# Optimization experiments

Hardware: AMD Instinct MI355X
Metric: run time of the kernel (lower is better)

Reference implementation:

```python
import jax, jax.numpy as jnp
import numpy as np

N = 50000
E = 800000
IN_C, HID_C, OUT_C = 128, 128, 64


def setup_inputs() -> dict:
    key = jax.random.key(0)
    ks = jax.random.split(key, 8)
    x = jax.random.normal(ks[0], (N, IN_C), dtype=jnp.float32)
    edge_index = jax.random.randint(ks[1], (2, E), 0, N, dtype=jnp.int64)
    s = lambda fan_in: 1.0 / np.sqrt(fan_in)
    W1 = jax.random.uniform(ks[2], (HID_C, IN_C), jnp.float32, -s(IN_C), s(IN_C))
    b1 = jnp.zeros((HID_C,), jnp.float32)
    W2 = jax.random.uniform(ks[3], (HID_C, HID_C), jnp.float32, -s(HID_C), s(HID_C))
    b2 = jnp.zeros((HID_C,), jnp.float32)
    Wp = jax.random.uniform(ks[4], (OUT_C, HID_C), jnp.float32, -s(HID_C), s(HID_C))
    bp = jax.random.uniform(ks[5], (OUT_C,), jnp.float32, -s(HID_C), s(HID_C))
    return {"x": x, "edge_index": edge_index, "W1": W1, "b1": b1,
            "W2": W2, "b2": b2, "Wp": Wp, "bp": bp}


def _gcn_conv(x, W, b, src, dst, n):
    # PyG GCNConv: linear transform (no bias), add self-loops, symmetric
    # normalization D^-1/2 A_hat D^-1/2, scatter-add aggregation, then bias.
    h = x @ W.T                                   # [N, out]
    loop = jnp.arange(n, dtype=src.dtype)
    s = jnp.concatenate([src, loop])              # [E+N]
    d = jnp.concatenate([dst, loop])              # [E+N]
    deg = jax.ops.segment_sum(jnp.ones_like(d, dtype=h.dtype), d, num_segments=n)
    dinv = jnp.where(deg > 0, jax.lax.rsqrt(deg), 0.0)
    norm = dinv[s] * dinv[d]                      # [E+N]
    msg = h[s] * norm[:, None]                    # gather + scale
    out = jax.ops.segment_sum(msg, d, num_segments=n)  # scatter-add to targets
    return out + b


def reference(x, edge_index, W1, b1, W2, b2, Wp, bp):
    src, dst = edge_index[0], edge_index[1]
    n = x.shape[0]
    h = jax.nn.relu(_gcn_conv(x, W1, b1, src, dst, n))
    h = jax.nn.relu(_gcn_conv(h, W2, b2, src, dst, n))
    out = h @ Wp.T + bp
    return jax.nn.relu(out)  # activation='relu'
```

## Files before the change

kernel.cpp:

```cpp
#include <hip/hip_runtime.h>

#define NN 50000
#define NE 800000
#define KD 128
#define NBUK 196
#define CHUNK 2048
#define SLACK 8192

typedef __attribute__((ext_vector_type(8))) short short8;
typedef __attribute__((ext_vector_type(4))) float f32x4;
typedef __attribute__((ext_vector_type(4))) unsigned short us4;

__device__ inline void splitbf(float x, short& h, short& l) {
    unsigned int u = __float_as_uint(x);
    unsigned int r = u + 0x8000u;
    short hh = (short)(r >> 16);
    float hf = __uint_as_float(((unsigned int)(unsigned short)hh) << 16);
    float lo = x - hf;
    unsigned int u2 = __float_as_uint(lo) + 0x8000u;
    h = hh;
    l = (short)(u2 >> 16);
}
__device__ inline unsigned short f2bf(float x) {
    unsigned int u = __float_as_uint(x);
    unsigned int r = u + 0x7FFFu + ((u >> 16) & 1u);
    return (unsigned short)(r >> 16);
}
__device__ inline float bf2f(unsigned short b) {
    return __uint_as_float(((unsigned int)b) << 16);
}

__global__ __launch_bounds__(256) void wsplit_k(
    const float* __restrict__ W1, const float* __restrict__ W2, const float* __restrict__ Wp,
    unsigned short* __restrict__ Wh, unsigned short* __restrict__ Wl,
    int* __restrict__ bcur)
{
    int t = threadIdx.x;
    if (blockIdx.x == 0 && t < NBUK) bcur[t] = 0;
    int i = blockIdx.x * 256 + t;
    float w;
    if (i < 16384) w = W1[i];
    else if (i < 32768) w = W2[i - 16384];
    else w = Wp[i - 32768];
    short h, l;
    splitbf(w, h, l);
    Wh[i] = (unsigned short)h;
    Wl[i] = (unsigned short)l;
}

__global__ __launch_bounds__(256) void bscat_k(const int* __restrict__ src, const int* __restrict__ dst,
    int* __restrict__ bcur, unsigned int* __restrict__ pairs, int e)
{
    __shared__ int h[NBUK], base[NBUK], cur[NBUK];
    int t = threadIdx.x;
    int e0 = blockIdx.x * CHUNK, e1 = min(e0 + CHUNK, e);
    for (int i = t; i < NBUK; i += 256) { h[i] = 0; cur[i] = 0; }
    __syncthreads();
    for (int i = e0 + t; i < e1; i += 256) atomicAdd(&h[dst[i] >> 8], 1);
    __syncthreads();
    for (int i = t; i < NBUK; i += 256) base[i] = h[i] ? atomicAdd(&bcur[i], h[i]) : 0;
    __syncthreads();
    for (int i = e0 + t; i < e1; i += 256) {
        int d = dst[i];
        int b = d >> 8;
        int r = atomicAdd(&cur[b], 1);
        pairs[(size_t)b * SLACK + base[b] + r] = (unsigned)src[i] | ((unsigned)(d & 255) << 16);
    }
}
__global__ __launch_bounds__(256) void bbuild_k(const unsigned int* __restrict__ pairs,
    const int* __restrict__ bcur,
    int* __restrict__ beg, int* __restrict__ endp, float* __restrict__ dinv,
    int* __restrict__ col)
{
    __shared__ int h[256], cur[256], exc[256], sh[256];
    int b = blockIdx.x, t = threadIdx.x;
    int nb = bcur[b];
    size_t rb = (size_t)b * SLACK;
    int d0 = b << 8;
    int nd = NN - d0; if (nd > 256) nd = 256;
    h[t] = 0; cur[t] = 0;
    __syncthreads();
    for (int i = t; i < nb; i += 256) atomicAdd(&h[(pairs[rb + i] >> 16) & 255], 1);
    __syncthreads();
    int v = h[t];
    sh[t] = v; __syncthreads();
    for (int off = 1; off < 256; off <<= 1) {
        int u = (t >= off) ? sh[t - off] : 0;
        __syncthreads();
        sh[t] += u;
        __syncthreads();
    }
    int ex = sh[t] - v;
    exc[t] = ex;
    if (t < nd) {
        beg[d0 + t]  = (int)rb + ex;
        endp[d0 + t] = (int)rb + ex + v;
        dinv[d0 + t] = rsqrtf(1.0f + (float)v);
    }
    __syncthreads();
    for (int i = t; i < nb; i += 256) {
        unsigned p = pairs[rb + i];
        int dl = (p >> 16) & 255;
        int r = atomicAdd(&cur[dl], 1);
        col[rb + exc[dl] + r] = (int)(p & 0xFFFFu);
    }
}

template<int CO, bool XBF, int EPI>
__global__ __launch_bounds__(256) void mgemm_k(
    const void* __restrict__ Xin,
    const unsigned short* __restrict__ Wh, const unsigned short* __restrict__ Wl,
    const float* __restrict__ dinv,
    const float* __restrict__ bout, void* __restrict__ outAv)
{
    __shared__ short8 WhV[CO * 16];
    __shared__ short8 WlV[CO * 16];

    const int t = threadIdx.x;

    for (int i = t; i < CO * 16; i += 256) {
        int c = i >> 4, G = i & 15;
        short8 h = *(const short8*)(Wh + c * KD + G * 8);
        short8 l = *(const short8*)(Wl + c * KD + G * 8);
        int Gs = G ^ (c & 15);
        WhV[c * 16 + Gs] = h;
        WlV[c * 16 + Gs] = l;
    }
    __syncthreads();

    const int wv = t >> 6, l = t & 63, q = l >> 4, lr = l & 15;
    const int row0 = blockIdx.x * 64 + wv * 16;
    constexpr int NCT = CO / 16;

    f32x4 acc[NCT];
#pragma unroll
    for (int ct = 0; ct < NCT; ++ct) acc[ct] = (f32x4){0.f, 0.f, 0.f, 0.f};

    int xrow = row0 + lr; if (xrow > NN - 1) xrow = NN - 1;

#pragma unroll
    for (int kk = 0; kk < 4; ++kk) {
        short8 ah, al;
        if (XBF) {
            ah = *(const short8*)((const unsigned short*)Xin + (size_t)xrow * KD + q * 8 + kk * 32);
        } else {
            const float* xbase = (const float*)Xin + (size_t)xrow * KD + q * 8 + kk * 32;
            float4 x0 = *(const float4*)xbase;
            float4 x1 = *(const float4*)(xbase + 4);
            float xs[8] = {x0.x, x0.y, x0.z, x0.w, x1.x, x1.y, x1.z, x1.w};
#pragma unroll
            for (int j = 0; j < 8; ++j) { short hh, ll; splitbf(xs[j], hh, ll); ah[j] = hh; al[j] = ll; }
        }

#pragma unroll
        for (int ct = 0; ct < NCT; ++ct) {
            int c = ct * 16 + lr;
            int Gs = (kk * 4 + q) ^ (c & 15);
            short8 bh = WhV[c * 16 + Gs];
            short8 bl = WlV[c * 16 + Gs];
            acc[ct] = __builtin_amdgcn_mfma_f32_16x16x32_bf16(ah, bh, acc[ct], 0, 0, 0);
            acc[ct] = __builtin_amdgcn_mfma_f32_16x16x32_bf16(ah, bl, acc[ct], 0, 0, 0);
            if (!XBF)
                acc[ct] = __builtin_amdgcn_mfma_f32_16x16x32_bf16(al, bh, acc[ct], 0, 0, 0);
        }
    }

    float dv[4]; int rok[4];
#pragma unroll
    for (int r = 0; r < 4; ++r) {
        int row = row0 + q * 4 + r;
        rok[r] = (row < NN);
        dv[r] = (EPI == 0 && rok[r]) ? dinv[row] : 0.f;
    }
#pragma unroll
    for (int ct = 0; ct < NCT; ++ct) {
        int c = ct * 16 + lr;
        float bc = (EPI == 1) ? bout[c] : 0.f;
#pragma unroll
        for (int r = 0; r < 4; ++r) {
            int row = row0 + q * 4 + r;
            if (rok[r]) {
                float v = acc[ct][r];
                if (EPI == 0) {
                    ((unsigned short*)outAv)[(size_t)row * CO + c] = f2bf(v * dv[r]);
                } else {
                    ((float*)outAv)[(size_t)row * CO + c] = fmaxf(0.f, v + bc);
                }
            }
        }
    }
}

__global__ __launch_bounds__(256) void gather_k(
    const unsigned short* __restrict__ Hs, unsigned short* __restrict__ outX,
    const int* __restrict__ begp, const int* __restrict__ endpp,
    const int* __restrict__ col,
    const float* __restrict__ dinv, const float* __restrict__ bias)
{
    int wave = threadIdx.x >> 6;
    int lane = threadIdx.x & 63;
    int h  = lane >> 5;
    int sl = lane & 31;
    int d = blockIdx.x * 4 + wave;
    if (d >= NN) return;
    int beg = begp[d], end = endpp[d];

    const unsigned short* hp = Hs + sl * 4;
    float4 bb = *(const float4*)(bias + sl * 4);

    float4 a0 = make_float4(0.f, 0.f, 0.f, 0.f);
    float4 a1 = make_float4(0.f, 0.f, 0.f, 0.f);
    float4 a2 = make_float4(0.f, 0.f, 0.f, 0.f);
    float4 a3 = make_float4(0.f, 0.f, 0.f, 0.f);

    if (h == 0) {
        us4 v = *(const us4*)(hp + (size_t)d * KD);
        a0.x = bf2f(v[0]); a0.y = bf2f(v[1]); a0.z = bf2f(v[2]); a0.w = bf2f(v[3]);
    }

    int j = beg + h;
    for (; j + 6 < end; j += 8) {
        int s0 = col[j],     s1 = col[j + 2];
        int s2 = col[j + 4], s3 = col[j + 6];
        us4 v0 = *(const us4*)(hp + (size_t)s0 * KD);
        us4 v1 = *(const us4*)(hp + (size_t)s1 * KD);
        us4 v2 = *(const us4*)(hp + (size_t)s2 * KD);
        us4 v3 = *(const us4*)(hp + (size_t)s3 * KD);
        a0.x += bf2f(v0[0]); a0.y += bf2f(v0[1]); a0.z += bf2f(v0[2]); a0.w += bf2f(v0[3]);
        a1.x += bf2f(v1[0]); a1.y += bf2f(v1[1]); a1.z += bf2f(v1[2]); a1.w += bf2f(v1[3]);
        a2.x += bf2f(v2[0]); a2.y += bf2f(v2[1]); a2.z += bf2f(v2[2]); a2.w += bf2f(v2[3]);
        a3.x += bf2f(v3[0]); a3.y += bf2f(v3[1]); a3.z += bf2f(v3[2]); a3.w += bf2f(v3[3]);
    }
    for (; j < end; j += 2) {
        int s = col[j];
        us4 v = *(const us4*)(hp + (size_t)s * KD);
        a0.x += bf2f(v[0]); a0.y += bf2f(v[1]); a0.z += bf2f(v[2]); a0.w += bf2f(v[3]);
    }

    float4 tt;
    tt.x = (a0.x + a1.x) + (a2.x + a3.x);
    tt.y = (a0.y + a1.y) + (a2.y + a3.y);
    tt.z = (a0.z + a1.z) + (a2.z + a3.z);
    tt.w = (a0.w + a1.w) + (a2.w + a3.w);
    tt.x += __shfl_xor(tt.x, 32);
    tt.y += __shfl_xor(tt.y, 32);
    tt.z += __shfl_xor(tt.z, 32);
    tt.w += __shfl_xor(tt.w, 32);

    if (h == 0) {
        float dvv = dinv[d];
        us4 r;
        r[0] = f2bf(fmaxf(0.f, tt.x * dvv + bb.x));
        r[1] = f2bf(fmaxf(0.f, tt.y * dvv + bb.y));
        r[2] = f2bf(fmaxf(0.f, tt.z * dvv + bb.z));
        r[3] = f2bf(fmaxf(0.f, tt.w * dvv + bb.w));
        *(us4*)(outX + (size_t)d * KD + sl * 4) = r;
    }
}

extern "C" void kernel_launch(void* const* d_in, const int* in_sizes, int n_in,
                              void* d_out, int out_size, void* d_ws, size_t ws_size,
                              hipStream_t stream) {
    const float* x    = (const float*)d_in[0];
    const int*   ei   = (const int*)d_in[1];
    const float* W1   = (const float*)d_in[2];
    const float* b1   = (const float*)d_in[3];
    const float* W2   = (const float*)d_in[4];
    const float* b2   = (const float*)d_in[5];
    const float* Wp   = (const float*)d_in[6];
    const float* bp   = (const float*)d_in[7];
    float* out = (float*)d_out;

    const int* esrc = ei;
    const int* edst = ei + NE;

    unsigned short* A  = (unsigned short*)d_ws;
    unsigned short* X2 = A + (size_t)NN * KD;
    float* dinv   = (float*)(X2 + (size_t)NN * KD);
    int*   beg    = (int*)(dinv + NN);
    int*   endp   = beg + NN;
    int*   col    = endp + NN;
    unsigned int* pairs = (unsigned int*)(col + NBUK * SLACK);
    int*   bcur   = (int*)(pairs + (size_t)NBUK * SLACK);
    unsigned short* Wh = (unsigned short*)(bcur + NBUK);
    unsigned short* Wl = Wh + 40960;

    const int NCH = (NE + CHUNK - 1) / CHUNK;

    wsplit_k<<<160, 256, 0, stream>>>(W1, W2, Wp, Wh, Wl, bcur);
    bscat_k <<<NCH, 256, 0, stream>>>(esrc, edst, bcur, pairs, NE);
    bbuild_k<<<NBUK, 256, 0, stream>>>(pairs, bcur, beg, endp, dinv, col);

    const int GB = (NN + 63) / 64;
    const int AB = (NN + 3) / 4;

    mgemm_k<128, false, 0><<<GB, 256, 0, stream>>>(x, Wh, Wl, dinv, nullptr, A);
    gather_k<<<AB, 256, 0, stream>>>(A, X2, beg, endp, col, dinv, b1);
    mgemm_k<128, true, 0><<<GB, 256, 0, stream>>>(X2, Wh + 16384, Wl + 16384, dinv, nullptr, A);
    gather_k<<<AB, 256, 0, stream>>>(A, X2, beg, endp, col, dinv, b2);
    mgemm_k<64, true, 1><<<GB, 256, 0, stream>>>(X2, Wh + 32768, Wl + 32768, dinv, bp, out);
}
```

Measured before the change: 164.0 us.

## Fuse neighbor gather aggregation with following GEMM through shared memory

Merges each gather kernel with the next layer's MFMA GEMM. A block aggregates 64 destination rows into a swizzled LDS tile, then multiplies that tile by the weights directly. This removes the X2 round trip through global memory and two kernel launches. In exchange, each wave walks 16 rows serially, so there is less parallelism and latency hiding in the gather, and weights are now read from global/L1 rather than staged in LDS.

```diff
diff --git a/kernel.cpp b/kernel.cpp
--- a/kernel.cpp
+++ b/kernel.cpp
@@ -106,13 +106,12 @@
     }
 }
 
-template<int CO, bool XBF, int EPI>
-__global__ __launch_bounds__(256) void mgemm_k(
-    const void* __restrict__ Xin,
+__global__ __launch_bounds__(256) void mgemm1_k(
+    const float* __restrict__ Xin,
     const unsigned short* __restrict__ Wh, const unsigned short* __restrict__ Wl,
-    const float* __restrict__ dinv,
-    const float* __restrict__ bout, void* __restrict__ outAv)
-{
+    const float* __restrict__ dinv, unsigned short* __restrict__ outA)
+{
+    constexpr int CO = 128;
     __shared__ short8 WhV[CO * 16];
     __shared__ short8 WlV[CO * 16];
 
@@ -140,17 +139,13 @@
 
 #pragma unroll
     for (int kk = 0; kk < 4; ++kk) {
+        const float* xbase = Xin + (size_t)xrow * KD + q * 8 + kk * 32;
+        float4 x0 = *(const float4*)xbase;
+        float4 x1 = *(const float4*)(xbase + 4);
+        float xs[8] = {x0.x, x0.y, x0.z, x0.w, x1.x, x1.y, x1.z, x1.w};
         short8 ah, al;
-        if (XBF) {
-            ah = *(const short8*)((const unsigned short*)Xin + (size_t)xrow * KD + q * 8 + kk * 32);
-        } else {
-            const float* xbase = (const float*)Xin + (size_t)xrow * KD + q * 8 + kk * 32;
-            float4 x0 = *(const float4*)xbase;
-            float4 x1 = *(const float4*)(xbase + 4);
-            float xs[8] = {x0.x, x0.y, x0.z, x0.w, x1.x, x1.y, x1.z, x1.w};
-#pragma unroll
-            for (int j = 0; j < 8; ++j) { short hh, ll; splitbf(xs[j], hh, ll); ah[j] = hh; al[j] = ll; }
-        }
+#pragma unroll
+        for (int j = 0; j < 8; ++j) { short hh, ll; splitbf(xs[j], hh, ll); ah[j] = hh; al[j] = ll; }
 
 #pragma unroll
         for (int ct = 0; ct < NCT; ++ct) {
@@ -160,11 +155,130 @@
             short8 bl = WlV[c * 16 + Gs];
             acc[ct] = __builtin_amdgcn_mfma_f32_16x16x32_bf16(ah, bh, acc[ct], 0, 0, 0);
             acc[ct] = __builtin_amdgcn_mfma_f32_16x16x32_bf16(ah, bl, acc[ct], 0, 0, 0);
-            if (!XBF)
-                acc[ct] = __builtin_amdgcn_mfma_f32_16x16x32_bf16(al, bh, acc[ct], 0, 0, 0);
-        }
-    }
-
+            acc[ct] = __builtin_amdgcn_mfma_f32_16x16x32_bf16(al, bh, acc[ct], 0, 0, 0);
+        }
+    }
+
+    float dv[4]; int rok[4];
+#pragma unroll
+    for (int r = 0; r < 4; ++r) {
+        int row = row0 + q * 4 + r;
+        rok[r] = (row < NN);
+        dv[r] = rok[r] ? dinv[row] : 0.f;
+    }
+#pragma unroll
+    for (int ct = 0; ct < NCT; ++ct) {
+        int c = ct * 16 + lr;
+#pragma unroll
+        for (int r = 0; r < 4; ++r) {
+            int row = row0 + q * 4 + r;
+            if (rok[r]) outA[(size_t)row * CO + c] = f2bf(acc[ct][r] * dv[r]);
+        }
+    }
+}
+
+template<int CO, int EPI>
+__global__ __launch_bounds__(256) void gg_k(
+    const unsigned short* __restrict__ Hs,
+    const int* __restrict__ begp, const int* __restrict__ endpp,
+    const int* __restrict__ col,
+    const float* __restrict__ dinv, const float* __restrict__ bias,
+    const unsigned short* __restrict__ Wh, const unsigned short* __restrict__ Wl,
+    const float* __restrict__ bout, void* __restrict__ outAv)
+{
+    __shared__ unsigned short Xs[64 * KD];
+
+    const int t = threadIdx.x;
+    const int wave = t >> 6, lane = t & 63;
+    const int h = lane >> 5, sl = lane & 31;
+    const int dbase = blockIdx.x * 64 + wave * 16;
+
+    const unsigned short* hp = Hs + sl * 4;
+    float4 bb = *(const float4*)(bias + sl * 4);
+
+    for (int it = 0; it < 16; ++it) {
+        int d = dbase + it;
+        bool ok = (d < NN);
+        int beg = 0, end = 0;
+        if (ok) { beg = begp[d]; end = endpp[d]; }
+
+        float4 a0 = make_float4(0.f, 0.f, 0.f, 0.f);
+        float4 a1 = make_float4(0.f, 0.f, 0.f, 0.f);
+        float4 a2 = make_float4(0.f, 0.f, 0.f, 0.f);
+        float4 a3 = make_float4(0.f, 0.f, 0.f, 0.f);
+
+        if (ok && h == 0) {
+            us4 v = *(const us4*)(hp + (size_t)d * KD);
+            a0.x = bf2f(v[0]); a0.y = bf2f(v[1]); a0.z = bf2f(v[2]); a0.w = bf2f(v[3]);
+        }
+
+        int j = beg + h;
+        for (; j + 6 < end; j += 8) {
+            int s0 = col[j],     s1 = col[j + 2];
+            int s2 = col[j + 4], s3 = col[j + 6];
+            us4 v0 = *(const us4*)(hp + (size_t)s0 * KD);
+            us4 v1 = *(const us4*)(hp + (size_t)s1 * KD);
+            us4 v2 = *(const us4*)(hp + (size_t)s2 * KD);
+            us4 v3 = *(const us4*)(hp + (size_t)s3 * KD);
+            a0.x += bf2f(v0[0]); a0.y += bf2f(v0[1]); a0.z += bf2f(v0[2]); a0.w += bf2f(v0[3]);
+            a1.x += bf2f(v1[0]); a1.y += bf2f(v1[1]); a1.z += bf2f(v1[2]); a1.w += bf2f(v1[3]);
+            a2.x += bf2f(v2[0]); a2.y += bf2f(v2[1]); a2.z += bf2f(v2[2]); a2.w += bf2f(v2[3]);
+            a3.x += bf2f(v3[0]); a3.y += bf2f(v3[1]); a3.z += bf2f(v3[2]); a3.w += bf2f(v3[3]);
+        }
+        for (; j < end; j += 2) {
+            int s = col[j];
+            us4 v = *(const us4*)(hp + (size_t)s * KD);
+            a0.x += bf2f(v[0]); a0.y += bf2f(v[1]); a0.z += bf2f(v[2]); a0.w += bf2f(v[3]);
+        }
+
+        float4 tt;
+        tt.x = (a0.x + a1.x) + (a2.x + a3.x);
+        tt.y = (a0.y + a1.y) + (a2.y + a3.y);
+        tt.z = (a0.z + a1.z) + (a2.z + a3.z);
+        tt.w = (a0.w + a1.w) + (a2.w + a3.w);
+        tt.x += __shfl_xor(tt.x, 32);
+        tt.y += __shfl_xor(tt.y, 32);
+        tt.z += __shfl_xor(tt.z, 32);
+        tt.w += __shfl_xor(tt.w, 32);
+
+        if (h == 0) {
+            float dvv = ok ? dinv[d] : 0.f;
+            us4 r;
+            r[0] = f2bf(fmaxf(0.f, tt.x * dvv + bb.x));
+            r[1] = f2bf(fmaxf(0.f, tt.y * dvv + bb.y));
+            r[2] = f2bf(fmaxf(0.f, tt.z * dvv + bb.z));
+            r[3] = f2bf(fmaxf(0.f, tt.w * dvv + bb.w));
+            int rl = wave * 16 + it;
+            int gs = (sl >> 1) ^ (rl & 15);
+            *(us4*)(Xs + rl * KD + gs * 8 + (sl & 1) * 4) = r;
+        }
+    }
+    __syncthreads();
+
+    const int q = lane >> 4, lr = lane & 15;
+    constexpr int NCT = CO / 16;
+
+    f32x4 acc[NCT];
+#pragma unroll
+    for (int ct = 0; ct < NCT; ++ct) acc[ct] = (f32x4){0.f, 0.f, 0.f, 0.f};
+
+    const int rl = wave * 16 + lr;
+
+#pragma unroll
+    for (int kk = 0; kk < 4; ++kk) {
+        int G = kk * 4 + q;
+        short8 ah = *(const short8*)(Xs + rl * KD + (G ^ lr) * 8);
+#pragma unroll
+        for (int ct = 0; ct < NCT; ++ct) {
+            int c = ct * 16 + lr;
+            short8 bh = *(const short8*)(Wh + c * KD + G * 8);
+            short8 bl = *(const short8*)(Wl + c * KD + G * 8);
+            acc[ct] = __builtin_amdgcn_mfma_f32_16x16x32_bf16(ah, bh, acc[ct], 0, 0, 0);
+            acc[ct] = __builtin_amdgcn_mfma_f32_16x16x32_bf16(ah, bl, acc[ct], 0, 0, 0);
+        }
+    }
+
+    const int row0 = blockIdx.x * 64 + wave * 16;
     float dv[4]; int rok[4];
 #pragma unroll
     for (int r = 0; r < 4; ++r) {
@@ -188,73 +302,6 @@
                 }
             }
         }
-    }
-}
-
-__global__ __launch_bounds__(256) void gather_k(
-    const unsigned short* __restrict__ Hs, unsigned short* __restrict__ outX,
-    const int* __restrict__ begp, const int* __restrict__ endpp,
-    const int* __restrict__ col,
-    const float* __restrict__ dinv, const float* __restrict__ bias)
-{
-    int wave = threadIdx.x >> 6;
-    int lane = threadIdx.x & 63;
-    int h  = lane >> 5;
-    int sl = lane & 31;
-    int d = blockIdx.x * 4 + wave;
-    if (d >= NN) return;
-    int beg = begp[d], end = endpp[d];
-
-    const unsigned short* hp = Hs + sl * 4;
-    float4 bb = *(const float4*)(bias + sl * 4);
-
-    float4 a0 = make_float4(0.f, 0.f, 0.f, 0.f);
-    float4 a1 = make_float4(0.f, 0.f, 0.f, 0.f);
-    float4 a2 = make_float4(0.f, 0.f, 0.f, 0.f);
-    float4 a3 = make_float4(0.f, 0.f, 0.f, 0.f);
-
-    if (h == 0) {
-        us4 v = *(const us4*)(hp + (size_t)d * KD);
-        a0.x = bf2f(v[0]); a0.y = bf2f(v[1]); a0.z = bf2f(v[2]); a0.w = bf2f(v[3]);
-    }
-
-    int j = beg + h;
-    for (; j + 6 < end; j += 8) {
-        int s0 = col[j],     s1 = col[j + 2];
-        int s2 = col[j + 4], s3 = col[j + 6];
-        us4 v0 = *(const us4*)(hp + (size_t)s0 * KD);
-        us4 v1 = *(const us4*)(hp + (size_t)s1 * KD);
-        us4 v2 = *(const us4*)(hp + (size_t)s2 * KD);
-        us4 v3 = *(const us4*)(hp + (size_t)s3 * KD);
-        a0.x += bf2f(v0[0]); a0.y += bf2f(v0[1]); a0.z += bf2f(v0[2]); a0.w += bf2f(v0[3]);
-        a1.x += bf2f(v1[0]); a1.y += bf2f(v1[1]); a1.z += bf2f(v1[2]); a1.w += bf2f(v1[3]);
-        a2.x += bf2f(v2[0]); a2.y += bf2f(v2[1]); a2.z += bf2f(v2[2]); a2.w += bf2f(v2[3]);
-        a3.x += bf2f(v3[0]); a3.y += bf2f(v3[1]); a3.z += bf2f(v3[2]); a3.w += bf2f(v3[3]);
-    }
-    for (; j < end; j += 2) {
-        int s = col[j];
-        us4 v = *(const us4*)(hp + (size_t)s * KD);
-        a0.x += bf2f(v[0]); a0.y += bf2f(v[1]); a0.z += bf2f(v[2]); a0.w += bf2f(v[3]);
-    }
-
-    float4 tt;
-    tt.x = (a0.x + a1.x) + (a2.x + a3.x);
-    tt.y = (a0.y + a1.y) + (a2.y + a3.y);
-    tt.z = (a0.z + a1.z) + (a2.z + a3.z);
-    tt.w = (a0.w + a1.w) + (a2.w + a3.w);
-    tt.x += __shfl_xor(tt.x, 32);
-    tt.y += __shfl_xor(tt.y, 32);
-    tt.z += __shfl_xor(tt.z, 32);
-    tt.w += __shfl_xor(tt.w, 32);
-
-    if (h == 0) {
-        float dvv = dinv[d];
-        us4 r;
-        r[0] = f2bf(fmaxf(0.f, tt.x * dvv + bb.x));
-        r[1] = f2bf(fmaxf(0.f, tt.y * dvv + bb.y));
-        r[2] = f2bf(fmaxf(0.f, tt.z * dvv + bb.z));
-        r[3] = f2bf(fmaxf(0.f, tt.w * dvv + bb.w));
-        *(us4*)(outX + (size_t)d * KD + sl * 4) = r;
     }
 }
 
@@ -275,8 +322,8 @@
     const int* edst = ei + NE;
 
     unsigned short* A  = (unsigned short*)d_ws;
-    unsigned short* X2 = A + (size_t)NN * KD;
-    float* dinv   = (float*)(X2 + (size_t)NN * KD);
+    unsigned short* A2 = A + (size_t)NN * KD;
+    float* dinv   = (float*)(A2 + (size_t)NN * KD);
     int*   beg    = (int*)(dinv + NN);
     int*   endp   = beg + NN;
     int*   col    = endp + NN;
@@ -286,17 +333,15 @@
     unsigned short* Wl = Wh + 40960;
 
     const int NCH = (NE + CHUNK - 1) / CHUNK;
+    const int GB  = (NN + 63) / 64;
 
     wsplit_k<<<160, 256, 0, stream>>>(W1, W2, Wp, Wh, Wl, bcur);
     bscat_k <<<NCH, 256, 0, stream>>>(esrc, edst, bcur, pairs, NE);
     bbuild_k<<<NBUK, 256, 0, stream>>>(pairs, bcur, beg, endp, dinv, col);
 
-    const int GB = (NN + 63) / 64;
-    const int AB = (NN + 3) / 4;
-
-    mgemm_k<128, false, 0><<<GB, 256, 0, stream>>>(x, Wh, Wl, dinv, nullptr, A);
-    gather_k<<<AB, 256, 0, stream>>>(A, X2, beg, endp, col, dinv, b1);
-    mgemm_k<128, true, 0><<<GB, 256, 0, stream>>>(X2, Wh + 16384, Wl + 16384, dinv, nullptr, A);
-    gather_k<<<AB, 256, 0, stream>>>(A, X2, beg, endp, col, dinv, b2);
-    mgemm_k<64, true, 1><<<GB, 256, 0, stream>>>(X2, Wh + 32768, Wl + 32768, dinv, bp, out);
-}
+    mgemm1_k<<<GB, 256, 0, stream>>>(x, Wh, Wl, dinv, A);
+    gg_k<128, 0><<<GB, 256, 0, stream>>>(A, beg, endp, col, dinv, b1,
+                                         Wh + 16384, Wl + 16384, nullptr, A2);
+    gg_k<64, 1><<<GB, 256, 0, stream>>>(A2, beg, endp, col, dinv, b2,
+                                        Wh + 32768, Wl + 32768, bp, out);
+}
```

Measured after the change: 230.9 us. 1.41x slower.
